# Optimization experiments

Hardware: AMD Instinct MI355X
Metric: run time of the kernel (lower is better)

The kernel has to match this reference:

```python
import jax, jax.numpy as jnp
import numpy as np

SCALE = 4
A = -0.75


def _bicubic_kernels():
    # cubic convolution coefficient matrix (Keys, a=-0.75), matching the torch module
    cubic = np.array([[0.0, A, -2.0 * A, A],
                      [1.0, 0.0, -(A + 3.0), A + 2.0],
                      [0.0, -A, 2.0 * A + 3.0, -(A + 2.0)],
                      [0.0, 0.0, A, -A]], dtype=np.float32)
    rows = []
    for d in range(SCALE):
        sv = np.float32(d) / np.float32(SCALE)
        rows.append(cubic @ np.array([1.0, sv, sv ** 2, sv ** 3], dtype=np.float32))
    return jnp.asarray(np.stack(rows))  # [s, 4] tap weights per sub-pixel phase


def setup_inputs() -> dict:
    key = jax.random.key(0)
    x = jax.random.normal(key, (16, 3, 256, 256), dtype=jnp.float32)
    return {"x": x, "kernels": _bicubic_kernels()}


def reference(x, kernels):
    n, c, h, w = x.shape
    s = kernels.shape[0]  # scale factor
    # replicate pad: (left=1, right=2, top=1, bottom=2)
    xp = jnp.pad(x, ((0, 0), (0, 0), (1, 2), (1, 2)), mode='edge')  # [n,c,h+3,w+3]
    wp = w + 3
    # vertical pass: 4-tap weighted sum over height, producing s phases per row
    win = jnp.stack([xp[:, :, j:j + h, :] for j in range(4)], axis=-1)  # [n,c,h,w+3,4]
    out = jnp.einsum('nchwj,kj->nchkw', win, kernels)  # [n,c,h,s,w+3]
    out = out.reshape(n, c, h * s, wp)  # interleave phases along height
    # horizontal pass: 4-tap weighted sum over width, s phases per column
    win = jnp.stack([out[:, :, :, j:j + w] for j in range(4)], axis=-1)  # [n,c,h*s,w,4]
    out = jnp.einsum('nchwj,kj->nchwk', win, kernels)  # [n,c,h*s,w,s]
    return out.reshape(n, c, h * s, w * s)
```

## Files before the change

### kernel.cpp

```cpp
#include <hip/hip_runtime.h>

#define H  256
#define W  256
#define S  4
#define OH (H * S)
#define OW (W * S)

__global__ __launch_bounds__(256) void bicubic_up4(
    const float* __restrict__ x, const float* __restrict__ kern,
    float* __restrict__ out)
{
    const int iw  = threadIdx.x;
    const int ihb = blockIdx.x * 4;
    const int nc  = blockIdx.y;

    float kk[16];
#pragma unroll
    for (int i = 0; i < 16; ++i) kk[i] = kern[i];

    const float* __restrict__ xp = x + (size_t)nc * (H * W);

    const int c0 = max(iw - 1, 0);
    const int c2 = min(iw + 1, W - 1);
    const int c3 = min(iw + 2, W - 1);
    const int cc[4] = { c0, iw, c2, c3 };

    float p[7][4];
#pragma unroll
    for (int t = 0; t < 7; ++t) {
        int r = ihb - 1 + t;
        r = r < 0 ? 0 : (r > H - 1 ? H - 1 : r);
        const float* row = xp + r * W;
#pragma unroll
        for (int i = 0; i < 4; ++i) p[t][i] = row[cc[i]];
    }

    float* __restrict__ obase =
        out + ((size_t)nc * OH + (size_t)ihb * S) * OW + (size_t)iw * S;

#pragma unroll
    for (int q = 0; q < 4; ++q) {
#pragma unroll
        for (int kv = 0; kv < 4; ++kv) {
            const float w0 = kk[kv * 4 + 0];
            const float w1 = kk[kv * 4 + 1];
            const float w2 = kk[kv * 4 + 2];
            const float w3 = kk[kv * 4 + 3];
            const float v0 = p[q][0]*w0 + p[q+1][0]*w1 + p[q+2][0]*w2 + p[q+3][0]*w3;
            const float v1 = p[q][1]*w0 + p[q+1][1]*w1 + p[q+2][1]*w2 + p[q+3][1]*w3;
            const float v2 = p[q][2]*w0 + p[q+1][2]*w1 + p[q+2][2]*w2 + p[q+3][2]*w3;
            const float v3 = p[q][3]*w0 + p[q+1][3]*w1 + p[q+2][3]*w2 + p[q+3][3]*w3;
            float4 o;
            o.x = v0*kk[0]  + v1*kk[1]  + v2*kk[2]  + v3*kk[3];
            o.y = v0*kk[4]  + v1*kk[5]  + v2*kk[6]  + v3*kk[7];
            o.z = v0*kk[8]  + v1*kk[9]  + v2*kk[10] + v3*kk[11];
            o.w = v0*kk[12] + v1*kk[13] + v2*kk[14] + v3*kk[15];
            *reinterpret_cast<float4*>(obase + ((size_t)q * S + kv) * OW) = o;
        }
    }
}

extern "C" void kernel_launch(void* const* d_in, const int* in_sizes, int n_in,
                              void* d_out, int out_size, void* d_ws, size_t ws_size,
                              hipStream_t stream) {
    const float* x    = (const float*)d_in[0];
    const float* kern = (const float*)d_in[1];
    float* out        = (float*)d_out;

    dim3 grid(H / 4, 16 * 3);
    dim3 block(256);
    bicubic_up4<<<grid, block, 0, stream>>>(x, kern, out);
}
```

Baseline: 202.2 us.

## Do horizontal pass first, vectorize interior loads, use nontemporal output stores

Reorders the separable filter so the horizontal 4-tap pass is applied to the 7 input rows once, and the vertical pass then produces each output float4 directly. This cuts per-output arithmetic compared with recomputing the column filter for every output row. Interior threads fetch their four neighbouring pixels with one unaligned vector load instead of four scalar loads. Output float4 writes become nontemporal stores, which aims to keep the large write stream from polluting caches. The reordering changes floating-point summation order slightly.

```diff
diff --git a/kernel.cpp b/kernel.cpp
--- a/kernel.cpp
+++ b/kernel.cpp
@@ -5,6 +5,9 @@
 #define S  4
 #define OH (H * S)
 #define OW (W * S)
+
+typedef float f32x4 __attribute__((ext_vector_type(4)));
+typedef f32x4 __attribute__((aligned(4))) f32x4_u;
 
 __global__ __launch_bounds__(256) void bicubic_up4(
     const float* __restrict__ x, const float* __restrict__ kern,
@@ -20,19 +23,28 @@
 
     const float* __restrict__ xp = x + (size_t)nc * (H * W);
 
+    const bool interior = (iw >= 1) && (iw <= W - 3);
     const int c0 = max(iw - 1, 0);
     const int c2 = min(iw + 1, W - 1);
     const int c3 = min(iw + 2, W - 1);
-    const int cc[4] = { c0, iw, c2, c3 };
 
-    float p[7][4];
+    float hb[7][4];
 #pragma unroll
     for (int t = 0; t < 7; ++t) {
         int r = ihb - 1 + t;
         r = r < 0 ? 0 : (r > H - 1 ? H - 1 : r);
-        const float* row = xp + r * W;
+        const float* __restrict__ row = xp + r * W;
+        float a, b, c, d;
+        if (interior) {
+            f32x4 v = *reinterpret_cast<const f32x4_u*>(row + (iw - 1));
+            a = v.x; b = v.y; c = v.z; d = v.w;
+        } else {
+            a = row[c0]; b = row[iw]; c = row[c2]; d = row[c3];
+        }
 #pragma unroll
-        for (int i = 0; i < 4; ++i) p[t][i] = row[cc[i]];
+        for (int ph = 0; ph < 4; ++ph)
+            hb[t][ph] = a * kk[ph * 4 + 0] + b * kk[ph * 4 + 1]
+                      + c * kk[ph * 4 + 2] + d * kk[ph * 4 + 3];
     }
 
     float* __restrict__ obase =
@@ -46,16 +58,13 @@
             const float w1 = kk[kv * 4 + 1];
             const float w2 = kk[kv * 4 + 2];
             const float w3 = kk[kv * 4 + 3];
-            const float v0 = p[q][0]*w0 + p[q+1][0]*w1 + p[q+2][0]*w2 + p[q+3][0]*w3;
-            const float v1 = p[q][1]*w0 + p[q+1][1]*w1 + p[q+2][1]*w2 + p[q+3][1]*w3;
-            const float v2 = p[q][2]*w0 + p[q+1][2]*w1 + p[q+2][2]*w2 + p[q+3][2]*w3;
-            const float v3 = p[q][3]*w0 + p[q+1][3]*w1 + p[q+2][3]*w2 + p[q+3][3]*w3;
-            float4 o;
-            o.x = v0*kk[0]  + v1*kk[1]  + v2*kk[2]  + v3*kk[3];
-            o.y = v0*kk[4]  + v1*kk[5]  + v2*kk[6]  + v3*kk[7];
-            o.z = v0*kk[8]  + v1*kk[9]  + v2*kk[10] + v3*kk[11];
-            o.w = v0*kk[12] + v1*kk[13] + v2*kk[14] + v3*kk[15];
-            *reinterpret_cast<float4*>(obase + ((size_t)q * S + kv) * OW) = o;
+            f32x4 o;
+            o.x = hb[q][0]*w0 + hb[q+1][0]*w1 + hb[q+2][0]*w2 + hb[q+3][0]*w3;
+            o.y = hb[q][1]*w0 + hb[q+1][1]*w1 + hb[q+2][1]*w2 + hb[q+3][1]*w3;
+            o.z = hb[q][2]*w0 + hb[q+1][2]*w1 + hb[q+2][2]*w2 + hb[q+3][2]*w3;
+            o.w = hb[q][3]*w0 + hb[q+1][3]*w1 + hb[q+2][3]*w2 + hb[q+3][3]*w3;
+            __builtin_nontemporal_store(
+                o, reinterpret_cast<f32x4*>(obase + ((size_t)(q * S + kv)) * OW));
         }
     }
 }
```

New measurement: 213.4 us. 1.06x slower.
